# Kernel tuning notes

Measured on AMD Instinct MI355X. Metric: run time of the kernel, lower is better.

Reference implementation:

```python
import jax, jax.numpy as jnp
import numpy as np

# Static config matching init_kwargs
NUM_EXPERTS = 8
CAP_FACTOR = 1.0
MIN_CAP = 8


def setup_inputs() -> dict:
    key = jax.random.key(0)
    ks = jax.random.split(key, 10)
    G, S, D, H, E = 4, 4096, 1024, 4096, NUM_EXPERTS
    s = 0.02  # init stddev like nn.initializers.normal(0.02)
    return {
        "x": jax.random.normal(ks[0], (G, S, D), dtype=jnp.float32),
        "gate": jax.random.normal(ks[1], (D, E), dtype=jnp.float32) * s,
        "W1": jax.random.normal(ks[2], (E, D, H), dtype=jnp.float32) * s,
        "b1": jnp.zeros((E, H), dtype=jnp.float32),
        "W2": jax.random.normal(ks[3], (E, H, D), dtype=jnp.float32) * s,
        "b2": jnp.zeros((E, D), dtype=jnp.float32),
        "Ws1": jax.random.normal(ks[4], (D, H), dtype=jnp.float32) * s,
        "bs1": jnp.zeros((H,), dtype=jnp.float32),
        "Ws2": jax.random.normal(ks[5], (H, D), dtype=jnp.float32) * s,
        "bs2": jnp.zeros((D,), dtype=jnp.float32),
    }


def reference(x, gate, W1, b1, W2, b2, Ws1, bs1, Ws2, bs2):
    G, S, D = x.shape
    E = gate.shape[1]
    T = G * S
    capacity = max(MIN_CAP, int(CAP_FACTOR * T / E))  # static -> 2048

    # ---- Router (inference path: indices + scores, loss = 0) ----
    logits = jnp.einsum('gsd,de->gse', x, gate)           # (G,S,E)
    probs = jax.nn.softmax(logits, axis=-1)
    flat_probs = probs.transpose(2, 0, 1).reshape(E, T)    # (E,T)
    # capacity <= T here, so padding width is 0 (kept implicit)
    scores, token_idx = jax.lax.top_k(flat_probs, k=capacity)  # (E,C)
    scores = jnp.where(scores > -1e8, scores, 0.0)

    # ---- Routed experts: gather -> per-expert FFN (grouped GEMM) -> scatter-add
    flat_x = x.reshape(T, D)
    tok = flat_x[token_idx]                                # (E,C,D) gather
    h = jax.nn.gelu(jnp.einsum('ecd,edh->ech', tok, W1) + b1[:, None, :])
    out_tok = jnp.einsum('ech,ehd->ecd', h, W2) + b2[:, None, :]
    scaled = out_tok * scores[..., None]                   # weight by routing prob
    routed = jnp.zeros_like(flat_x).at[token_idx.reshape(-1)].add(
        scaled.reshape(E * capacity, D)).reshape(G, S, D)

    # ---- Shared expert (single FFN applied to all tokens) ----
    shared = jax.nn.gelu(jnp.einsum('gsd,dh->gsh', x, Ws1) + bs1)
    shared = jnp.einsum('gsh,hd->gsd', shared, Ws2) + bs2

    return routed + shared
```

## Files before the change

kernel.cpp:

```cpp
#include <hip/hip_runtime.h>
#include <hip/hip_bf16.h>

using bf16 = __hip_bfloat16;
typedef short v8s __attribute__((ext_vector_type(8)));
typedef float v4f __attribute__((ext_vector_type(4)));

#define NE 8
#define NT 16384
#define ND 1024
#define NH 4096
#define CAP 2048

__device__ __forceinline__ void load_lds16(const void* g, void* s) {
  __builtin_amdgcn_global_load_lds(
      (const __attribute__((address_space(1))) unsigned int*)g,
      (__attribute__((address_space(3))) unsigned int*)s, 16, 0, 0);
}

__device__ __forceinline__ float gelu_tanh(float x) {
  float u = 0.7978845608028654f * (x + 0.044715f * x * x * x);
  float e = __expf(2.0f * u);
  float t = 1.0f - 2.0f / (e + 1.0f);
  return 0.5f * x * (1.0f + t);
}

__global__ __launch_bounds__(256) void cvt_bf16(const float* __restrict__ s,
                                                bf16* __restrict__ d, int n) {
  for (int i = (blockIdx.x * 256 + threadIdx.x) * 4; i < n; i += gridDim.x * 1024) {
    float4 v = *(const float4*)(s + i);
    bf16 o[4];
    o[0] = __float2bfloat16(v.x); o[1] = __float2bfloat16(v.y);
    o[2] = __float2bfloat16(v.z); o[3] = __float2bfloat16(v.w);
    *(ushort4*)(d + i) = *(ushort4*)o;
  }
}

__global__ __launch_bounds__(256) void tcvt(const float* __restrict__ src,
                                            bf16* __restrict__ dst, int R, int C) {
  __shared__ float tile[32][33];
  size_t mo = (size_t)blockIdx.z * R * C;
  int c0 = blockIdx.x * 32, r0 = blockIdx.y * 32;
  int tx = threadIdx.x & 31, ty = threadIdx.x >> 5;
  for (int i = ty; i < 32; i += 8)
    tile[i][tx] = src[mo + (size_t)(r0 + i) * C + c0 + tx];
  __syncthreads();
  for (int i = ty; i < 32; i += 8)
    dst[mo + (size_t)(c0 + i) * R + r0 + tx] = __float2bfloat16(tile[tx][i]);
}

__global__ __launch_bounds__(256) void router_k(const float* __restrict__ x,
                                                const float* __restrict__ gate,
                                                float* __restrict__ probs) {
  int wave = threadIdx.x >> 6, lane = threadIdx.x & 63;
  int t = blockIdx.x * 4 + wave;
  const float* xr = x + (size_t)t * ND;
  double acc[NE];
#pragma unroll
  for (int e = 0; e < NE; e++) acc[e] = 0.0;
  for (int d = lane; d < ND; d += 64) {
    double xv = (double)xr[d];
    const float* g = gate + d * NE;
#pragma unroll
    for (int e = 0; e < NE; e++) acc[e] += xv * (double)g[e];
  }
#pragma unroll
  for (int e = 0; e < NE; e++) {
    double v = acc[e];
#pragma unroll
    for (int off = 32; off > 0; off >>= 1) v += __shfl_xor(v, off);
    acc[e] = v;
  }
  if (lane == 0) {
    float l[NE], m = -1e30f;
#pragma unroll
    for (int e = 0; e < NE; e++) { l[e] = (float)acc[e]; m = fmaxf(m, l[e]); }
    float p[NE], s = 0.f;
#pragma unroll
    for (int e = 0; e < NE; e++) { p[e] = expf(l[e] - m); s += p[e]; }
#pragma unroll
    for (int e = 0; e < NE; e++) probs[e * NT + t] = p[e] / s;
  }
}

__global__ __launch_bounds__(1024) void topk_k(const float* __restrict__ probs,
                                               unsigned* __restrict__ thr_key,
                                               int* __restrict__ needed) {
  int e = blockIdx.x;
  const float* p = probs + e * NT;
  __shared__ int hist[256];
  __shared__ unsigned s_pref;
  __shared__ int s_rank;
  unsigned prefix = 0;
  int rank = CAP;
  for (int rd = 0; rd < 4; rd++) {
    int shift = 24 - rd * 8;
    if (threadIdx.x < 256) hist[threadIdx.x] = 0;
    __syncthreads();
    unsigned mask = (rd == 0) ? 0u : (0xFFFFFFFFu << (shift + 8));
    for (int t = threadIdx.x; t < NT; t += 1024) {
      unsigned k = __float_as_uint(p[t]);
      if ((k & mask) == prefix) atomicAdd(&hist[(k >> shift) & 255], 1);
    }
    __syncthreads();
    if (threadIdx.x == 0) {
      int cum = 0, b = 255;
      for (;;) {
        int c = hist[b];
        if (cum + c >= rank || b == 0) break;
        cum += c; b--;
      }
      s_pref = prefix | ((unsigned)b << shift);
      s_rank = rank - cum;
    }
    __syncthreads();
    prefix = s_pref; rank = s_rank;
    __syncthreads();
  }
  if (threadIdx.x == 0) { thr_key[e] = prefix; needed[e] = rank; }
}

__global__ void zero_counters(int* p) {
  if (threadIdx.x < 2 * NE) p[threadIdx.x] = 0;
}

__global__ __launch_bounds__(256) void compact_k(const float* __restrict__ probs,
                                                 const unsigned* __restrict__ thr_key,
                                                 const int* __restrict__ needed,
                                                 int* __restrict__ cnt, int* __restrict__ eqc,
                                                 int* __restrict__ tok, float* __restrict__ scr) {
  int gid = blockIdx.x * 256 + threadIdx.x;
  int e = gid >> 14, t = gid & (NT - 1);
  float pv = probs[gid];
  unsigned k = __float_as_uint(pv);
  unsigned thr = thr_key[e];
  int nd = needed[e];
  bool gt = k > thr, eq = k == thr;
  unsigned long long mgt = __ballot(gt), meq = __ballot(eq);
  int lane = threadIdx.x & 63, wv = threadIdx.x >> 6;
  __shared__ int wcnt[2][4];
  __shared__ int base[2];
  if (lane == 0) { wcnt[0][wv] = __popcll(mgt); wcnt[1][wv] = __popcll(meq); }
  __syncthreads();
  if (threadIdx.x == 0) {
    int s0 = wcnt[0][0] + wcnt[0][1] + wcnt[0][2] + wcnt[0][3];
    int s1 = wcnt[1][0] + wcnt[1][1] + wcnt[1][2] + wcnt[1][3];
    base[0] = s0 ? atomicAdd(&cnt[e], s0) : 0;
    base[1] = s1 ? atomicAdd(&eqc[e], s1) : 0;
  }
  __syncthreads();
  unsigned long long lm = (1ull << lane) - 1ull;
  if (gt) {
    int p = __popcll(mgt & lm);
    for (int w = 0; w < wv; w++) p += wcnt[0][w];
    int slot = base[0] + p;
    tok[e * CAP + slot] = t; scr[e * CAP + slot] = pv;
  } else if (eq) {
    int q = base[1] + __popcll(meq & lm);
    for (int w = 0; w < wv; w++) q += wcnt[1][w];
    if (q < nd) {
      int slot = (CAP - nd) + q;
      tok[e * CAP + slot] = t; scr[e * CAP + slot] = pv;
    }
  }
}

#define BAR() __builtin_amdgcn_s_barrier()

template <int MODE>
__global__ __launch_bounds__(512, 2) void gemm256(
    const bf16* __restrict__ A, int lda, const int* __restrict__ rowmap,
    const bf16* __restrict__ BT, long long bstride, int gshift,
    const float* __restrict__ bias, int bias_stride,
    int N, int K,
    bf16* __restrict__ outH, float* __restrict__ outF,
    const int* __restrict__ tok, const float* __restrict__ scr) {
  __shared__ __attribute__((aligned(16))) char A0s[32768];
  __shared__ __attribute__((aligned(16))) char A1s[32768];
  __shared__ __attribute__((aligned(16))) char B0s[32768];
  __shared__ __attribute__((aligned(16))) char B1s[32768];
  const int tid = threadIdx.x;
  const int lane = tid & 63, wv = tid >> 6;
  const int wr = wv >> 2, wc = wv & 3;
  const int m0 = blockIdx.y << 8, n0 = blockIdx.x << 8;
  const int grp = m0 >> gshift;
  const bf16* Bp = BT + (size_t)grp * (size_t)bstride;
  const float* bp = bias + (size_t)grp * (size_t)bias_stride;
  const int nt = K >> 6;

  const int srow = tid >> 3;
  const int pc = tid & 7;
  const int gc = pc ^ (srow & 7);
  const bf16* srcA[4]; const bf16* srcB[4];
#pragma unroll
  for (int g = 0; g < 4; g++) {
    int am = m0 + g * 64 + srow;
    int ar = rowmap ? rowmap[am] : am;
    srcA[g] = A + (size_t)ar * lda + gc * 8;
    srcB[g] = Bp + (size_t)(n0 + g * 64 + srow) * K + gc * 8;
  }
#define STA(ARR, T, H)                                                        \
  { char* d_ = (ARR) + (H) * 16384 + tid * 16;                                \
    load_lds16(srcA[(H) * 2 + 0] + (size_t)(T) * 64, d_);                     \
    load_lds16(srcA[(H) * 2 + 1] + (size_t)(T) * 64, d_ + 8192); }
#define STB(ARR, T, H)                                                        \
  { char* d_ = (ARR) + (H) * 16384 + tid * 16;                                \
    load_lds16(srcB[(H) * 2 + 0] + (size_t)(T) * 64, d_);                     \
    load_lds16(srcB[(H) * 2 + 1] + (size_t)(T) * 64, d_ + 8192); }

  const int fr = lane & 15, hi = lane >> 4;
  const int xr = fr & 7;
  const int cb0 = ((0 + hi) ^ xr) << 4;
  const int cb1 = ((4 + hi) ^ xr) << 4;
  const int arow = ((wr << 7) + fr) << 7;
  const int brow = ((wc << 6) + fr) << 7;

  v4f acc[8][4] = {};
  v8s a[4][2], b01[2][2], b23[2][2];

#define R_AL(BASE)                                                            \
  _Pragma("unroll") for (int mi = 0; mi < 4; mi++) {                          \
    a[mi][0] = *(const v8s*)((BASE) + arow + mi * 2048 + cb0);                \
    a[mi][1] = *(const v8s*)((BASE) + arow + mi * 2048 + cb1);                \
  }
#define R_AH(BASE)                                                            \
  _Pragma("unroll") for (int mi = 0; mi < 4; mi++) {                          \
    a[mi][0] = *(const v8s*)((BASE) + arow + (4 + mi) * 2048 + cb0);          \
    a[mi][1] = *(const v8s*)((BASE) + arow + (4 + mi) * 2048 + cb1);          \
  }
#define R_B01(BASE)                                                           \
  _Pragma("unroll") for (int ni = 0; ni < 2; ni++) {                          \
    b01[ni][0] = *(const v8s*)((BASE) + brow + ni * 2048 + cb0);              \
    b01[ni][1] = *(const v8s*)((BASE) + brow + ni * 2048 + cb1);              \
  }
#define R_B23(BASE)                                                           \
  _Pragma("unroll") for (int ni = 0; ni < 2; ni++) {                          \
    b23[ni][0] = *(const v8s*)((BASE) + brow + (2 + ni) * 2048 + cb0);        \
    b23[ni][1] = *(const v8s*)((BASE) + brow + (2 + ni) * 2048 + cb1);        \
  }
#define MFMA_Q(BB, MOFF, NOFF)                                                \
  __builtin_amdgcn_s_setprio(1);                                              \
  _Pragma("unroll") for (int kk = 0; kk < 2; kk++)                            \
  _Pragma("unroll") for (int mi = 0; mi < 4; mi++)                            \
  _Pragma("unroll") for (int ni = 0; ni < 2; ni++)                            \
    acc[(MOFF) + mi][(NOFF) + ni] = __builtin_amdgcn_mfma_f32_16x16x32_bf16(  \
        a[mi][kk], BB[ni][kk], acc[(MOFF) + mi][(NOFF) + ni], 0, 0, 0);       \
  __builtin_amdgcn_s_setprio(0);

#define BODY(AR, BR, AN, T)                                                   \
  {                                                                           \
    R_AL(AR); R_B01(BR);                                                      \
    STA(AN, (T) + 1, 0);                                                      \
    BAR();                                                                    \
    MFMA_Q(b01, 0, 0);                                                        \
    BAR();                                                                    \
    R_B23(BR);                                                                \
    STA(AN, (T) + 1, 1);                                                      \
    BAR();                                                                    \
    MFMA_Q(b23, 0, 2);                                                        \
    BAR();                                                                    \
    R_AH(AR);                                                                 \
    STB(BR, (T) + 2, 0);                                                      \
    BAR();                                                                    \
    MFMA_Q(b01, 4, 0);                                                        \
    BAR();                                                                    \
    STB(BR, (T) + 2, 1);                                                      \
    asm volatile("s_waitcnt vmcnt(4)" ::: "memory");                          \
    BAR();                                                                    \
    MFMA_Q(b23, 4, 2);                                                        \
    BAR();                                                                    \
  }

  STA(A0s, 0, 0); STA(A0s, 0, 1);
  STB(B0s, 0, 0); STB(B0s, 0, 1);
  STB(B1s, 1, 0); STB(B1s, 1, 1);
  asm volatile("s_waitcnt vmcnt(4)" ::: "memory");
  BAR();

  for (int t = 0; t < nt; t += 2) {
    BODY(A0s, B0s, A1s, t);
    BODY(A1s, B1s, A0s, t + 1);
  }
  asm volatile("s_waitcnt vmcnt(0) lgkmcnt(0)" ::: "memory");

  float bv[4];
#pragma unroll
  for (int ni = 0; ni < 4; ni++) bv[ni] = bp[n0 + (wc << 6) + ni * 16 + fr];
  const int rbase = m0 + (wr << 7) + (hi << 2);
#pragma unroll
  for (int mi = 0; mi < 8; mi++) {
#pragma unroll
    for (int r = 0; r < 4; r++) {
      int gm = rbase + mi * 16 + r;
      int trow = 0; float sv = 0.f;
      if (MODE == 2) { trow = tok[gm]; sv = scr[gm]; }
#pragma unroll
      for (int ni = 0; ni < 4; ni++) {
        int gn = n0 + (wc << 6) + ni * 16 + fr;
        float v = acc[mi][ni][r] + bv[ni];
        if (MODE == 0)      outH[(size_t)gm * N + gn] = __float2bfloat16(gelu_tanh(v));
        else if (MODE == 1) outF[(size_t)gm * N + gn] = v;
        else                atomicAdd(outF + (size_t)trow * N + gn, v * sv);
      }
    }
  }
}

extern "C" void kernel_launch(void* const* d_in, const int* in_sizes, int n_in,
                              void* d_out, int out_size, void* d_ws, size_t ws_size,
                              hipStream_t stream) {
  const float* x   = (const float*)d_in[0];
  const float* gate= (const float*)d_in[1];
  const float* W1  = (const float*)d_in[2];
  const float* b1  = (const float*)d_in[3];
  const float* W2  = (const float*)d_in[4];
  const float* b2  = (const float*)d_in[5];
  const float* Ws1 = (const float*)d_in[6];
  const float* bs1 = (const float*)d_in[7];
  const float* Ws2 = (const float*)d_in[8];
  const float* bs2 = (const float*)d_in[9];
  float* out = (float*)d_out;

  char* w = (char*)d_ws;
  size_t off = 0;
  auto alloc = [&](size_t bytes) {
    void* p = w + off;
    off = (off + bytes + 255) & ~(size_t)255;
    return p;
  };
  bf16* xb    = (bf16*)alloc((size_t)NT * ND * 2);
  bf16* w1T   = (bf16*)alloc((size_t)NE * NH * ND * 2);
  bf16* w2T   = (bf16*)alloc((size_t)NE * ND * NH * 2);
  bf16* ws1T  = (bf16*)alloc((size_t)NH * ND * 2);
  bf16* ws2T  = (bf16*)alloc((size_t)ND * NH * 2);
  bf16* h     = (bf16*)alloc((size_t)NT * NH * 2);
  float* probs= (float*)alloc((size_t)NE * NT * 4);
  unsigned* thr = (unsigned*)alloc(NE * 4);
  int* needed = (int*)alloc(NE * 4);
  int* cnt    = (int*)alloc(2 * NE * 4);
  int* eqc    = cnt + NE;
  int* tok    = (int*)alloc((size_t)NE * CAP * 4);
  float* scr  = (float*)alloc((size_t)NE * CAP * 4);
  (void)alloc(65536);
  if (off > ws_size) return;

  cvt_bf16<<<2048, 256, 0, stream>>>(x, xb, NT * ND);
  tcvt<<<dim3(NH / 32, ND / 32, NE), 256, 0, stream>>>(W1, w1T, ND, NH);
  tcvt<<<dim3(ND / 32, NH / 32, NE), 256, 0, stream>>>(W2, w2T, NH, ND);
  tcvt<<<dim3(NH / 32, ND / 32, 1), 256, 0, stream>>>(Ws1, ws1T, ND, NH);
  tcvt<<<dim3(ND / 32, NH / 32, 1), 256, 0, stream>>>(Ws2, ws2T, NH, ND);

  router_k<<<NT / 4, 256, 0, stream>>>(x, gate, probs);
  topk_k<<<NE, 1024, 0, stream>>>(probs, thr, needed);
  zero_counters<<<1, 64, 0, stream>>>(cnt);
  compact_k<<<NE * NT / 256, 256, 0, stream>>>(probs, thr, needed, cnt, eqc, tok, scr);

  gemm256<0><<<dim3(NH / 256, NT / 256), 512, 0, stream>>>(
      xb, ND, nullptr, ws1T, 0, 30, bs1, 0, NH, ND, h, nullptr, nullptr, nullptr);
  gemm256<1><<<dim3(ND / 256, NT / 256), 512, 0, stream>>>(
      h, NH, nullptr, ws2T, 0, 30, bs2, 0, ND, NH, nullptr, out, nullptr, nullptr);

  gemm256<0><<<dim3(NH / 256, NT / 256), 512, 0, stream>>>(
      xb, ND, tok, w1T, (long long)NH * ND, 11, b1, NH, NH, ND, h, nullptr, nullptr, nullptr);
  gemm256<2><<<dim3(ND / 256, NT / 256), 512, 0, stream>>>(
      h, NH, nullptr, w2T, (long long)ND * NH, 11, b2, ND, ND, NH, nullptr, out, tok, scr);
}
```

Before: 942.5 us.

## Switch GEMM to 32x32x16 MFMA with two-phase pipelined loop body

Replaces the 16x16x32 bf16 MFMA tiling with 32x32x16 instructions, so each wave holds 4x2 accumulators of 16 floats and reads all B fragments once per K tile. The loop body drops from eight barriers to two, issuing both A-tile and both B-tile async loads per phase. A DRAIN template flag makes the gathered routed up-projection wait for all outstanding loads instead of allowing four in flight. This aims to cut LDS traffic and barrier overhead, at the cost of different register pressure and a changed epilogue row mapping.

After: 994.3 us. 1.06x slower.

```diff
diff --git a/kernel.cpp b/kernel.cpp
--- a/kernel.cpp
+++ b/kernel.cpp
@@ -3,7 +3,7 @@
 
 using bf16 = __hip_bfloat16;
 typedef short v8s __attribute__((ext_vector_type(8)));
-typedef float v4f __attribute__((ext_vector_type(4)));
+typedef float v16f __attribute__((ext_vector_type(16)));
 
 #define NE 8
 #define NT 16384
@@ -166,7 +166,7 @@
 
 #define BAR() __builtin_amdgcn_s_barrier()
 
-template <int MODE>
+template <int MODE, int DRAIN>
 __global__ __launch_bounds__(512, 2) void gemm256(
     const bf16* __restrict__ A, int lda, const int* __restrict__ rowmap,
     const bf16* __restrict__ BT, long long bstride, int gshift,
@@ -207,67 +207,49 @@
     load_lds16(srcB[(H) * 2 + 0] + (size_t)(T) * 64, d_);                     \
     load_lds16(srcB[(H) * 2 + 1] + (size_t)(T) * 64, d_ + 8192); }
 
-  const int fr = lane & 15, hi = lane >> 4;
-  const int xr = fr & 7;
-  const int cb0 = ((0 + hi) ^ xr) << 4;
-  const int cb1 = ((4 + hi) ^ xr) << 4;
-  const int arow = ((wr << 7) + fr) << 7;
-  const int brow = ((wc << 6) + fr) << 7;
-
-  v4f acc[8][4] = {};
-  v8s a[4][2], b01[2][2], b23[2][2];
-
-#define R_AL(BASE)                                                            \
-  _Pragma("unroll") for (int mi = 0; mi < 4; mi++) {                          \
-    a[mi][0] = *(const v8s*)((BASE) + arow + mi * 2048 + cb0);                \
-    a[mi][1] = *(const v8s*)((BASE) + arow + mi * 2048 + cb1);                \
-  }
-#define R_AH(BASE)                                                            \
-  _Pragma("unroll") for (int mi = 0; mi < 4; mi++) {                          \
-    a[mi][0] = *(const v8s*)((BASE) + arow + (4 + mi) * 2048 + cb0);          \
-    a[mi][1] = *(const v8s*)((BASE) + arow + (4 + mi) * 2048 + cb1);          \
-  }
-#define R_B01(BASE)                                                           \
-  _Pragma("unroll") for (int ni = 0; ni < 2; ni++) {                          \
-    b01[ni][0] = *(const v8s*)((BASE) + brow + ni * 2048 + cb0);              \
-    b01[ni][1] = *(const v8s*)((BASE) + brow + ni * 2048 + cb1);              \
-  }
-#define R_B23(BASE)                                                           \
-  _Pragma("unroll") for (int ni = 0; ni < 2; ni++) {                          \
-    b23[ni][0] = *(const v8s*)((BASE) + brow + (2 + ni) * 2048 + cb0);        \
-    b23[ni][1] = *(const v8s*)((BASE) + brow + (2 + ni) * 2048 + cb1);        \
-  }
-#define MFMA_Q(BB, MOFF, NOFF)                                                \
+  const int l31 = lane & 31, kh = lane >> 5, xr = lane & 7;
+  int coff[4];
+#pragma unroll
+  for (int s = 0; s < 4; s++) coff[s] = (((s << 1) + kh) ^ xr) << 4;
+  int offA[4];
+#pragma unroll
+  for (int mf = 0; mf < 4; mf++) offA[mf] = (((wr << 7) + (mf << 5) + l31) << 7);
+  int offB[2];
+#pragma unroll
+  for (int nf = 0; nf < 2; nf++) offB[nf] = (((wc << 6) + (nf << 5) + l31) << 7);
+
+  v16f acc[4][2] = {};
+  v8s a[4][2], b[2][4];
+
+#define R_AS(BASE, S0)                                                        \
+  _Pragma("unroll") for (int mf = 0; mf < 4; mf++)                            \
+  _Pragma("unroll") for (int ss = 0; ss < 2; ss++)                            \
+    a[mf][ss] = *(const v8s*)((BASE) + offA[mf] + coff[(S0) + ss]);
+#define R_BALL(BASE)                                                          \
+  _Pragma("unroll") for (int nf = 0; nf < 2; nf++)                            \
+  _Pragma("unroll") for (int s = 0; s < 4; s++)                               \
+    b[nf][s] = *(const v8s*)((BASE) + offB[nf] + coff[s]);
+#define MFMA_P(S0)                                                            \
   __builtin_amdgcn_s_setprio(1);                                              \
-  _Pragma("unroll") for (int kk = 0; kk < 2; kk++)                            \
-  _Pragma("unroll") for (int mi = 0; mi < 4; mi++)                            \
-  _Pragma("unroll") for (int ni = 0; ni < 2; ni++)                            \
-    acc[(MOFF) + mi][(NOFF) + ni] = __builtin_amdgcn_mfma_f32_16x16x32_bf16(  \
-        a[mi][kk], BB[ni][kk], acc[(MOFF) + mi][(NOFF) + ni], 0, 0, 0);       \
+  _Pragma("unroll") for (int ss = 0; ss < 2; ss++)                            \
+  _Pragma("unroll") for (int mf = 0; mf < 4; mf++)                            \
+  _Pragma("unroll") for (int nf = 0; nf < 2; nf++)                            \
+    acc[mf][nf] = __builtin_amdgcn_mfma_f32_32x32x16_bf16(                    \
+        a[mf][ss], b[nf][(S0) + ss], acc[mf][nf], 0, 0, 0);                   \
   __builtin_amdgcn_s_setprio(0);
 
 #define BODY(AR, BR, AN, T)                                                   \
   {                                                                           \
-    R_AL(AR); R_B01(BR);                                                      \
-    STA(AN, (T) + 1, 0);                                                      \
+    R_AS(AR, 0); R_BALL(BR);                                                  \
+    STA(AN, (T) + 1, 0); STA(AN, (T) + 1, 1);                                 \
     BAR();                                                                    \
-    MFMA_Q(b01, 0, 0);                                                        \
+    MFMA_P(0);                                                                \
+    R_AS(AR, 2);                                                              \
+    STB(BR, (T) + 2, 0); STB(BR, (T) + 2, 1);                                 \
+    if (DRAIN) { asm volatile("s_waitcnt vmcnt(0)" ::: "memory"); }           \
+    else       { asm volatile("s_waitcnt vmcnt(4)" ::: "memory"); }           \
     BAR();                                                                    \
-    R_B23(BR);                                                                \
-    STA(AN, (T) + 1, 1);                                                      \
-    BAR();                                                                    \
-    MFMA_Q(b23, 0, 2);                                                        \
-    BAR();                                                                    \
-    R_AH(AR);                                                                 \
-    STB(BR, (T) + 2, 0);                                                      \
-    BAR();                                                                    \
-    MFMA_Q(b01, 4, 0);                                                        \
-    BAR();                                                                    \
-    STB(BR, (T) + 2, 1);                                                      \
-    asm volatile("s_waitcnt vmcnt(4)" ::: "memory");                          \
-    BAR();                                                                    \
-    MFMA_Q(b23, 4, 2);                                                        \
-    BAR();                                                                    \
+    MFMA_P(2);                                                                \
   }
 
   STA(A0s, 0, 0); STA(A0s, 0, 1);
@@ -282,21 +264,20 @@
   }
   asm volatile("s_waitcnt vmcnt(0) lgkmcnt(0)" ::: "memory");
 
-  float bv[4];
-#pragma unroll
-  for (int ni = 0; ni < 4; ni++) bv[ni] = bp[n0 + (wc << 6) + ni * 16 + fr];
-  const int rbase = m0 + (wr << 7) + (hi << 2);
-#pragma unroll
-  for (int mi = 0; mi < 8; mi++) {
-#pragma unroll
-    for (int r = 0; r < 4; r++) {
-      int gm = rbase + mi * 16 + r;
+  float bv[2];
+#pragma unroll
+  for (int nf = 0; nf < 2; nf++) bv[nf] = bp[n0 + (wc << 6) + (nf << 5) + l31];
+#pragma unroll
+  for (int mf = 0; mf < 4; mf++) {
+#pragma unroll
+    for (int reg = 0; reg < 16; reg++) {
+      int gm = m0 + (wr << 7) + (mf << 5) + (reg & 3) + ((reg >> 2) << 3) + (kh << 2);
       int trow = 0; float sv = 0.f;
       if (MODE == 2) { trow = tok[gm]; sv = scr[gm]; }
 #pragma unroll
-      for (int ni = 0; ni < 4; ni++) {
-        int gn = n0 + (wc << 6) + ni * 16 + fr;
-        float v = acc[mi][ni][r] + bv[ni];
+      for (int nf = 0; nf < 2; nf++) {
+        int gn = n0 + (wc << 6) + (nf << 5) + l31;
+        float v = acc[mf][nf][reg] + bv[nf];
         if (MODE == 0)      outH[(size_t)gm * N + gn] = __float2bfloat16(gelu_tanh(v));
         else if (MODE == 1) outF[(size_t)gm * N + gn] = v;
         else                atomicAdd(outF + (size_t)trow * N + gn, v * sv);
@@ -354,13 +335,13 @@
   zero_counters<<<1, 64, 0, stream>>>(cnt);
   compact_k<<<NE * NT / 256, 256, 0, stream>>>(probs, thr, needed, cnt, eqc, tok, scr);
 
-  gemm256<0><<<dim3(NH / 256, NT / 256), 512, 0, stream>>>(
+  gemm256<0, 0><<<dim3(NH / 256, NT / 256), 512, 0, stream>>>(
       xb, ND, nullptr, ws1T, 0, 30, bs1, 0, NH, ND, h, nullptr, nullptr, nullptr);
-  gemm256<1><<<dim3(ND / 256, NT / 256), 512, 0, stream>>>(
+  gemm256<1, 0><<<dim3(ND / 256, NT / 256), 512, 0, stream>>>(
       h, NH, nullptr, ws2T, 0, 30, bs2, 0, ND, NH, nullptr, out, nullptr, nullptr);
 
-  gemm256<0><<<dim3(NH / 256, NT / 256), 512, 0, stream>>>(
+  gemm256<0, 1><<<dim3(NH / 256, NT / 256), 512, 0, stream>>>(
       xb, ND, tok, w1T, (long long)NH * ND, 11, b1, NH, NH, ND, h, nullptr, nullptr, nullptr);
-  gemm256<2><<<dim3(ND / 256, NT / 256), 512, 0, stream>>>(
+  gemm256<2, 0><<<dim3(ND / 256, NT / 256), 512, 0, stream>>>(
       h, NH, nullptr, w2T, (long long)ND * NH, 11, b2, ND, ND, NH, nullptr, out, tok, scr);
 }
```
